# Kernel tuning notes

Measured on AMD Instinct MI355X. Metric: run time of the kernel, lower is better.

The kernel has to match this reference:

```python
import jax, jax.numpy as jnp
import numpy as np

NEG_SLOPE = 0.2  # PyG GATConv default leaky_relu slope


def _gat_layer(x, src, dst, n_nodes, W, a_src, a_dst, b, heads, out_ch):
    # x: [N, Fin] -> h: [N, H, C]
    h = (x @ W).reshape(n_nodes, heads, out_ch)
    alpha_s = jnp.einsum('nhc,hc->nh', h, a_src)  # [N, H]
    alpha_d = jnp.einsum('nhc,hc->nh', h, a_dst)  # [N, H]
    e = jax.nn.leaky_relu(alpha_s[src] + alpha_d[dst], NEG_SLOPE)  # [E, H]
    # segment softmax over edges grouped by destination node
    m = jax.ops.segment_max(e, dst, num_segments=n_nodes)          # [N, H]
    e = jnp.exp(e - m[dst])
    denom = jax.ops.segment_sum(e, dst, num_segments=n_nodes)      # [N, H]
    alpha = e / denom[dst]                                          # self-loops guarantee denom > 0
    msg = alpha[:, :, None] * h[src]                                # [E, H, C]
    out = jax.ops.segment_sum(msg, dst, num_segments=n_nodes)      # [N, H, C]
    return out.reshape(n_nodes, heads * out_ch) + b


def reference(x, edge_index, batch, W1, a_src1, a_dst1, b1, W2, a_src2, a_dst2, b2, fc_w, fc_b):
    n_nodes = x.shape[0]
    heads = a_src1.shape[0]
    # PyG GATConv adds self-loops by default
    loops = jnp.arange(n_nodes, dtype=edge_index.dtype)
    src = jnp.concatenate([edge_index[0], loops])
    dst = jnp.concatenate([edge_index[1], loops])

    h = _gat_layer(x, src, dst, n_nodes, W1, a_src1, a_dst1, b1, heads, 64)
    h = jax.nn.relu(h)  # dropout is identity in eval mode
    h = _gat_layer(h, src, dst, n_nodes, W2, a_src2, a_dst2, b2, heads, 16)
    h = jax.nn.relu(h)

    n_graphs = 64
    sums = jax.ops.segment_sum(h, batch, num_segments=n_graphs)                    # [G, 64]
    counts = jax.ops.segment_sum(jnp.ones((n_nodes,), h.dtype), batch, num_segments=n_graphs)
    pooled = sums / jnp.maximum(counts, 1.0)[:, None]                              # global_mean_pool
    return pooled @ fc_w + fc_b


def setup_inputs() -> dict:
    key = jax.random.key(0)
    ks = jax.random.split(key, 12)
    N, E, F_in, G = 50000, 800000, 128, 64
    H = 4
    x = jax.random.normal(ks[0], (N, F_in), jnp.float32)
    edge_index = jax.random.randint(ks[1], (2, E), 0, N, jnp.int32)
    batch = jnp.sort(jax.random.randint(ks[2], (N,), 0, G, jnp.int32))
    s1 = 1.0 / np.sqrt(F_in)
    s2 = 1.0 / np.sqrt(H * 64)
    s3 = 1.0 / np.sqrt(H * 16)
    return {
        'x': x,
        'edge_index': edge_index,
        'batch': batch,
        'W1': jax.random.normal(ks[3], (F_in, H * 64), jnp.float32) * s1,
        'a_src1': jax.random.normal(ks[4], (H, 64), jnp.float32) * s1,
        'a_dst1': jax.random.normal(ks[5], (H, 64), jnp.float32) * s1,
        'b1': jnp.zeros((H * 64,), jnp.float32),
        'W2': jax.random.normal(ks[6], (H * 64, H * 16), jnp.float32) * s2,
        'a_src2': jax.random.normal(ks[7], (H, 16), jnp.float32) * s2,
        'a_dst2': jax.random.normal(ks[8], (H, 16), jnp.float32) * s2,
        'b2': jnp.zeros((H * 16,), jnp.float32),
        'fc_w': jax.random.normal(ks[9], (H * 16, 32), jnp.float32) * s3,
        'fc_b': jnp.zeros((32,), jnp.float32),
    }
```

## Files before the change

### kernel.cpp

```cpp
#include <hip/hip_runtime.h>
#include <hip/hip_bf16.h>
#include <hip/hip_fp16.h>
#include <math.h>

#define HEADS 4
#define CAP 64
#define CS 16

typedef _Float16 half8_t __attribute__((ext_vector_type(8)));
typedef float float4_t __attribute__((ext_vector_type(4)));


__global__ __launch_bounds__(256) void prep_k(int* cnt, unsigned short* slots, int N, int NB,
                                              const float* __restrict__ W1, _Float16* __restrict__ W1T,
                                              const float* __restrict__ W2, _Float16* __restrict__ W2T) {
    int bx = blockIdx.x;
    if (bx < NB) {
        int i = bx * 256 + threadIdx.x;
        if (i < N) {
            cnt[(size_t)i * CS] = 1;
            slots[(size_t)i * CAP] = (unsigned short)i;
        }
    } else if (bx < NB + 128) {
        int k = bx - NB;
        int n = threadIdx.x;
        W1T[n * 128 + k] = (_Float16)W1[k * 256 + n];
    } else {
        int n = bx - NB - 128;
        int k = threadIdx.x;
        W2T[n * 256 + k] = (_Float16)W2[k * 64 + n];
    }
}


__global__ __launch_bounds__(256) void fused_scatter_gemm1_k(
    const int* __restrict__ src, const int* __restrict__ dst,
    int* __restrict__ cnt, unsigned short* __restrict__ slots, int E, int SB,
    const float* __restrict__ A,
    const _Float16* __restrict__ BT,
    __half* __restrict__ hout,
    const float* __restrict__ avs,
    const float* __restrict__ avd,
    float* __restrict__ os,
    float* __restrict__ od, int M) {
    __shared__ _Float16 lds[4 * 16 * 72];

    if ((int)blockIdx.x < SB) {
        int T = SB * 256;
        int t0 = blockIdx.x * 256 + threadIdx.x;
        int d[8], s[8];
        #pragma unroll
        for (int k = 0; k < 8; k++) {
            int i = t0 + k * T;
            if (i < E) { d[k] = dst[i]; s[k] = src[i]; }
            else d[k] = -1;
        }
        int p[8];
        #pragma unroll
        for (int k = 0; k < 8; k++) {
            if (d[k] >= 0) p[k] = atomicAdd(&cnt[(size_t)d[k] * CS], 1);
        }
        #pragma unroll
        for (int k = 0; k < 8; k++) {
            if (d[k] >= 0 && p[k] < CAP)
                slots[(size_t)d[k] * CAP + p[k]] = (unsigned short)s[k];
        }
        return;
    }

    int bx = blockIdx.x - SB;
    int wave = threadIdx.x >> 6;
    int lane = threadIdx.x & 63;
    int q = lane >> 4;
    int c16 = lane & 15;
    int row0 = bx * 64 + wave * 16;

    half8_t a[4];
    int ar = row0 + c16;
    bool avalid = (ar < M);
    const float* ap = A + (size_t)ar * 128;
    #pragma unroll
    for (int ks = 0; ks < 4; ks++) {
        if (avalid) {
            float4 f0 = *(const float4*)(ap + ks * 32 + q * 8);
            float4 f1 = *(const float4*)(ap + ks * 32 + q * 8 + 4);
            half8_t h;
            h[0] = (_Float16)f0.x; h[1] = (_Float16)f0.y;
            h[2] = (_Float16)f0.z; h[3] = (_Float16)f0.w;
            h[4] = (_Float16)f1.x; h[5] = (_Float16)f1.y;
            h[6] = (_Float16)f1.z; h[7] = (_Float16)f1.w;
            a[ks] = h;
        } else {
            a[ks] = (half8_t)(_Float16)0.0f;
        }
    }

    float4_t acc[16];
    #pragma unroll
    for (int ct = 0; ct < 16; ct++) acc[ct] = (float4_t)0.f;

    #pragma unroll
    for (int ks = 0; ks < 4; ks++) {
        #pragma unroll
        for (int ct = 0; ct < 16; ct++) {
            half8_t b = *(const half8_t*)(BT + (size_t)(ct * 16 + c16) * 128 + ks * 32 + q * 8);
            acc[ct] = __builtin_amdgcn_mfma_f32_16x16x32_f16(a[ks], b, acc[ct], 0, 0, 0);
        }
    }

    float psh[4][4] = {}, pdh[4][4] = {};
    #pragma unroll
    for (int ct = 0; ct < 16; ct++) {
        int h = ct >> 2;
        int cih = (ct & 3) * 16 + c16;
        float as_v = avs[h * 64 + cih];
        float ad_v = avd[h * 64 + cih];
        #pragma unroll
        for (int r = 0; r < 4; r++) {
            psh[h][r] = fmaf(acc[ct][r], as_v, psh[h][r]);
            pdh[h][r] = fmaf(acc[ct][r], ad_v, pdh[h][r]);
        }
    }
    #pragma unroll
    for (int h = 0; h < 4; h++) {
        #pragma unroll
        for (int r = 0; r < 4; r++) {
            #pragma unroll
            for (int o = 8; o >= 1; o >>= 1) {
                psh[h][r] += __shfl_down(psh[h][r], o, 16);
                pdh[h][r] += __shfl_down(pdh[h][r], o, 16);
            }
        }
    }
    if (c16 == 0) {
        #pragma unroll
        for (int r = 0; r < 4; r++) {
            int gr = row0 + q * 4 + r;
            if (gr < M) {
                #pragma unroll
                for (int h = 0; h < 4; h++) {
                    os[(size_t)gr * HEADS + h] = psh[h][r];
                    od[(size_t)gr * HEADS + h] = pdh[h][r];
                }
            }
        }
    }

    _Float16* wl = lds + wave * (16 * 72);
    #pragma unroll
    for (int chunk = 0; chunk < 4; chunk++) {
        #pragma unroll
        for (int c4 = 0; c4 < 4; c4++) {
            int ct = chunk * 4 + c4;
            #pragma unroll
            for (int r = 0; r < 4; r++) {
                wl[(q * 4 + r) * 72 + c4 * 16 + c16] = (_Float16)acc[ct][r];
            }
        }
        __syncthreads();
        #pragma unroll
        for (int pass = 0; pass < 2; pass++) {
            int idx8 = pass * 64 + lane;
            int row = idx8 >> 3;
            int col8 = idx8 & 7;
            int gr = row0 + row;
            if (gr < M) {
                *(half8_t*)(hout + (size_t)gr * 256 + chunk * 64 + col8 * 8) =
                    *(const half8_t*)(wl + row * 72 + col8 * 8);
            }
        }
        __syncthreads();
    }
}


__global__ __launch_bounds__(256) void mfma_gemm2_k(
    const _Float16* __restrict__ Ah,
    const _Float16* __restrict__ BT,
    __half* __restrict__ hout,
    const float* __restrict__ avs,
    const float* __restrict__ avd,
    float* __restrict__ os,
    float* __restrict__ od, int M) {
    __shared__ _Float16 lds[4 * 16 * 64];
    int wave = threadIdx.x >> 6;
    int lane = threadIdx.x & 63;
    int q = lane >> 4;
    int c16 = lane & 15;
    int row0 = blockIdx.x * 64 + wave * 16;

    half8_t a[8];
    int ar = row0 + c16;
    bool avalid = (ar < M);
    const _Float16* ap = Ah + (size_t)ar * 256;
    #pragma unroll
    for (int ks = 0; ks < 8; ks++) {
        if (avalid) a[ks] = *(const half8_t*)(ap + ks * 32 + q * 8);
        else        a[ks] = (half8_t)(_Float16)0.0f;
    }

    float4_t acc[4];
    #pragma unroll
    for (int ct = 0; ct < 4; ct++) acc[ct] = (float4_t)0.f;

    #pragma unroll
    for (int ks = 0; ks < 8; ks++) {
        #pragma unroll
        for (int ct = 0; ct < 4; ct++) {
            half8_t b = *(const half8_t*)(BT + (size_t)(ct * 16 + c16) * 256 + ks * 32 + q * 8);
            acc[ct] = __builtin_amdgcn_mfma_f32_16x16x32_f16(a[ks], b, acc[ct], 0, 0, 0);
        }
    }

    float ps[4][4], pd[4][4];
    #pragma unroll
    for (int ct = 0; ct < 4; ct++) {
        float as_v = avs[ct * 16 + c16];
        float ad_v = avd[ct * 16 + c16];
        #pragma unroll
        for (int r = 0; r < 4; r++) {
            ps[ct][r] = acc[ct][r] * as_v;
            pd[ct][r] = acc[ct][r] * ad_v;
            #pragma unroll
            for (int o = 8; o >= 1; o >>= 1) {
                ps[ct][r] += __shfl_down(ps[ct][r], o, 16);
                pd[ct][r] += __shfl_down(pd[ct][r], o, 16);
            }
        }
    }
    if (c16 == 0) {
        #pragma unroll
        for (int r = 0; r < 4; r++) {
            int gr = row0 + q * 4 + r;
            if (gr < M) {
                #pragma unroll
                for (int ct = 0; ct < 4; ct++) {
                    os[(size_t)gr * HEADS + ct] = ps[ct][r];
                    od[(size_t)gr * HEADS + ct] = pd[ct][r];
                }
            }
        }
    }

    _Float16* wl = lds + wave * (16 * 64);
    #pragma unroll
    for (int ct = 0; ct < 4; ct++) {
        #pragma unroll
        for (int r = 0; r < 4; r++) {
            wl[(q * 4 + r) * 64 + ct * 16 + c16] = (_Float16)acc[ct][r];
        }
    }
    __syncthreads();
    #pragma unroll
    for (int pass = 0; pass < 2; pass++) {
        int idx8 = pass * 64 + lane;
        int row = idx8 >> 3;
        int col8 = idx8 & 7;
        int gr = row0 + row;
        if (gr < M) {
            *(half8_t*)(hout + (size_t)gr * 64 + col8 * 8) =
                *(const half8_t*)(wl + row * 64 + col8 * 8);
        }
    }
}


__global__ __launch_bounds__(256) void gat_agg64_f16_k(
    const __half* __restrict__ hsrc,
    const float* __restrict__ as,
    const float* __restrict__ ad,
    const int* __restrict__ cnt,
    const unsigned short* __restrict__ slots,
    const float* __restrict__ bias,
    __half* __restrict__ outh,
    int N) {
    int node = blockIdx.x * 4 + (threadIdx.x >> 6);
    if (node >= N) return;
    int l = threadIdx.x & 63;
    int h = l >> 4;
    int je = l & 15;
    int hb = h << 4;
    int deg = min(cnt[(size_t)node * CS], CAP);
    const unsigned short* sp = slots + (size_t)node * CAP;
    float adh = ad[(size_t)node * HEADS + h];
    float4 bv = *(const float4*)(bias + l * 4);

    int sv[4];
    float ev[4];
    #pragma unroll
    for (int k = 0; k < 4; k++) {
        int j = k * 16 + je;
        sv[k] = (j < deg) ? (int)sp[j] : 0;
    }
    #pragma unroll
    for (int k = 0; k < 4; k++) {
        int j = k * 16 + je;
        if (j < deg) {
            float a = as[(size_t)sv[k] * HEADS + h] + adh;
            ev[k] = (a > 0.f) ? a : 0.2f * a;
        } else {
            ev[k] = -INFINITY;
        }
    }
    float m = fmaxf(fmaxf(ev[0], ev[1]), fmaxf(ev[2], ev[3]));
    #pragma unroll
    for (int o = 8; o >= 1; o >>= 1) m = fmaxf(m, __shfl_xor(m, o));
    float pv[4];
    float den = 0.f;
    #pragma unroll
    for (int k = 0; k < 4; k++) {
        pv[k] = (k * 16 + je < deg) ? __expf(ev[k] - m) : 0.f;
        den += pv[k];
    }
    #pragma unroll
    for (int o = 8; o >= 1; o >>= 1) den += __shfl_xor(den, o);

    float4 acc = make_float4(0.f, 0.f, 0.f, 0.f);
    #pragma unroll
    for (int k = 0; k < 4; k++) {
        int base = k * 16;
        if (base >= deg) break;
        int cl = min(16, deg - base);
        #pragma unroll
        for (int half = 0; half < 2; half++) {
            int j0 = half * 8;
            if (j0 >= cl) break;
            float pj[8]; int sj[8];
            #pragma unroll
            for (int jj = 0; jj < 8; jj++) {
                pj[jj] = __shfl(pv[k], hb + j0 + jj);
                sj[jj] = __shfl(sv[k], hb + j0 + jj);
            }
            uint2 rv[8];
            #pragma unroll
            for (int jj = 0; jj < 8; jj++) {
                if (j0 + jj < cl) rv[jj] = *(const uint2*)(hsrc + (size_t)sj[jj] * 256 + l * 4);
            }
            #pragma unroll
            for (int jj = 0; jj < 8; jj++) {
                if (j0 + jj < cl) {
                    float2 a0 = __half22float2(*(__half2*)&rv[jj].x);
                    float2 b0 = __half22float2(*(__half2*)&rv[jj].y);
                    acc.x = fmaf(pj[jj], a0.x, acc.x); acc.y = fmaf(pj[jj], a0.y, acc.y);
                    acc.z = fmaf(pj[jj], b0.x, acc.z); acc.w = fmaf(pj[jj], b0.y, acc.w);
                }
            }
        }
    }

    float inv = 1.f / den;
    float rx = fmaxf(fmaf(acc.x, inv, bv.x), 0.f);
    float ry = fmaxf(fmaf(acc.y, inv, bv.y), 0.f);
    float rz = fmaxf(fmaf(acc.z, inv, bv.z), 0.f);
    float rw = fmaxf(fmaf(acc.w, inv, bv.w), 0.f);
    __half2* op = (__half2*)(outh + (size_t)node * 256 + l * 4);
    op[0] = __floats2half2_rn(rx, ry);
    op[1] = __floats2half2_rn(rz, rw);
}


__global__ __launch_bounds__(256) void gat_agg16_f16_k(
    const __half* __restrict__ hsrc,
    const float* __restrict__ as,
    const float* __restrict__ ad,
    const int* __restrict__ cnt,
    const unsigned short* __restrict__ slots,
    const float* __restrict__ bias,
    float* __restrict__ out, int N) {
    int node = blockIdx.x * 4 + (threadIdx.x >> 6);
    if (node >= N) return;
    int l = threadIdx.x & 63;
    int ha = l >> 4;
    int je = l & 15;
    int q = l & 15;
    int hh = q >> 2;
    int eg = l >> 4;
    int deg = min(cnt[(size_t)node * CS], CAP);
    const unsigned short* sp = slots + (size_t)node * CAP;
    float adh = ad[(size_t)node * HEADS + ha];
    float m = -INFINITY, den = 0.f;
    float4 acc = make_float4(0.f, 0.f, 0.f, 0.f);
    for (int base = 0; base < deg; base += 16) {
        int cl = min(16, deg - base);
        int s = 0;
        float e = -INFINITY;
        if (je < cl) {
            s = sp[base + je];
            float a = as[(size_t)s * HEADS + ha] + adh;
            e = (a > 0.f) ? a : 0.2f * a;
        }
        float cmax = e;
        #pragma unroll
        for (int o = 8; o >= 1; o >>= 1) cmax = fmaxf(cmax, __shfl_xor(cmax, o));
        float m_new = fmaxf(m, cmax);
        float p = (je < cl) ? __expf(e - m_new) : 0.f;
        float sum = p;
        #pragma unroll
        for (int o = 8; o >= 1; o >>= 1) sum += __shfl_xor(sum, o);
        float sc = __expf(m - m_new);
        den = den * sc + sum;
        m = m_new;
        float sch = __shfl(sc, hh << 4);
        acc.x *= sch; acc.y *= sch; acc.z *= sch; acc.w *= sch;

        int jbase = eg * 4;
        float pj[4]; int sj[4]; bool vj[4];
        #pragma unroll
        for (int jj = 0; jj < 4; jj++) {
            int j = jbase + jj;
            int jc = min(j, cl - 1);
            pj[jj] = __shfl(p, (hh << 4) + jc);
            sj[jj] = __shfl(s, (hh << 4) + jc);
            vj[jj] = (j < cl);
        }
        uint2 rv[4];
        #pragma unroll
        for (int jj = 0; jj < 4; jj++) {
            if (vj[jj]) rv[jj] = *(const uint2*)(hsrc + (size_t)sj[jj] * 64 + q * 4);
        }
        #pragma unroll
        for (int jj = 0; jj < 4; jj++) {
            if (vj[jj]) {
                float2 f0 = __half22float2(*(__half2*)&rv[jj].x);
                float2 f1 = __half22float2(*(__half2*)&rv[jj].y);
                acc.x = fmaf(pj[jj], f0.x, acc.x); acc.y = fmaf(pj[jj], f0.y, acc.y);
                acc.z = fmaf(pj[jj], f1.x, acc.z); acc.w = fmaf(pj[jj], f1.y, acc.w);
            }
        }
    }
    acc.x += __shfl_xor(acc.x, 16); acc.y += __shfl_xor(acc.y, 16);
    acc.z += __shfl_xor(acc.z, 16); acc.w += __shfl_xor(acc.w, 16);
    acc.x += __shfl_xor(acc.x, 32); acc.y += __shfl_xor(acc.y, 32);
    acc.z += __shfl_xor(acc.z, 32); acc.w += __shfl_xor(acc.w, 32);
    float denh = __shfl(den, hh << 4);
    if (eg == 0) {
        float inv = 1.f / denh;
        float4 bv = *(const float4*)(bias + q * 4);
        float4 r;
        r.x = fmaxf(fmaf(acc.x, inv, bv.x), 0.f);
        r.y = fmaxf(fmaf(acc.y, inv, bv.y), 0.f);
        r.z = fmaxf(fmaf(acc.z, inv, bv.z), 0.f);
        r.w = fmaxf(fmaf(acc.w, inv, bv.w), 0.f);
        *(float4*)(out + (size_t)node * 64 + q * 4) = r;
    }
}


__global__ __launch_bounds__(256) void bounds_zero_k(const int* __restrict__ batch, int N,
                                                     int* __restrict__ bstart,
                                                     float* __restrict__ sums) {
    int t = threadIdx.x;
    if (t <= 64) {
        int lo = 0, hi = N;
        while (lo < hi) {
            int mid = (lo + hi) >> 1;
            if (batch[mid] < t) lo = mid + 1; else hi = mid;
        }
        bstart[t] = lo;
    }
    for (int i = t; i < 64 * 64; i += 256) sums[i] = 0.f;
}

__global__ __launch_bounds__(256) void pool_sum_k(const float* __restrict__ g2,
                                                  const int* __restrict__ batch,
                                                  float* __restrict__ sums, int N) {
    int c = threadIdx.x & 63;
    int r = threadIdx.x >> 6;
    int base = blockIdx.x * 256;
    int lim = min(base + 256, N);
    float acc = 0.f;
    int cur = -1;
    for (int n = base + r; n < lim; n += 4) {
        int g = batch[n];
        if (g != cur) {
            if (cur >= 0) atomicAdd(&sums[cur * 64 + c], acc);
            acc = 0.f;
            cur = g;
        }
        acc += g2[(size_t)n * 64 + c];
    }
    if (cur >= 0) atomicAdd(&sums[cur * 64 + c], acc);
}

__global__ void fc_k(const float* __restrict__ sums, const int* __restrict__ bstart,
                     const float* __restrict__ w, const float* __restrict__ b,
                     float* __restrict__ out) {
    int g = blockIdx.x, o = threadIdx.x;
    float cnt_ = (float)max(bstart[g + 1] - bstart[g], 1);
    float inv = 1.f / cnt_;
    float acc = b[o];
    for (int k = 0; k < 64; k++) acc = fmaf(sums[g * 64 + k] * inv, w[k * 32 + o], acc);
    out[g * 32 + o] = acc;
}


static inline size_t align_up(size_t x, size_t a) { return (x + a - 1) & ~(a - 1); }

extern "C" void kernel_launch(void* const* d_in, const int* in_sizes, int n_in,
                              void* d_out, int out_size, void* d_ws, size_t ws_size,
                              hipStream_t stream) {
    const float* x      = (const float*)d_in[0];
    const int*   ei     = (const int*)d_in[1];
    const int*   batch  = (const int*)d_in[2];
    const float* W1     = (const float*)d_in[3];
    const float* a_src1 = (const float*)d_in[4];
    const float* a_dst1 = (const float*)d_in[5];
    const float* b1     = (const float*)d_in[6];
    const float* W2     = (const float*)d_in[7];
    const float* a_src2 = (const float*)d_in[8];
    const float* a_dst2 = (const float*)d_in[9];
    const float* b2     = (const float*)d_in[10];
    const float* fc_w   = (const float*)d_in[11];
    const float* fc_b   = (const float*)d_in[12];
    float* out = (float*)d_out;

    const int N = in_sizes[2];
    const int E = in_sizes[1] / 2;
    const int F_in = in_sizes[0] / N;
    const int D1 = HEADS * 64;
    const int D2 = HEADS * 16;

    const int* src = ei;
    const int* dst = ei + E;

    char* w = (char*)d_ws;
    size_t off = 0;
    auto alloc = [&](size_t bytes) {
        size_t p = off;
        off = align_up(off + bytes, 256);
        return (void*)(w + p);
    };
    int* cnt    = (int*)alloc((size_t)N * CS * 4);
    unsigned short* slots = (unsigned short*)alloc((size_t)N * CAP * 2);
    int* bstart = (int*)alloc(65 * 4);
    float* pooled = (float*)alloc(64 * 64 * 4);
    float* as1  = (float*)alloc((size_t)N * HEADS * 4);
    float* ad1  = (float*)alloc((size_t)N * HEADS * 4);
    float* as2  = (float*)alloc((size_t)N * HEADS * 4);
    float* ad2  = (float*)alloc((size_t)N * HEADS * 4);
    __half* h1h = (__half*)alloc((size_t)N * D1 * 2);
    __half* g1h = (__half*)alloc((size_t)N * D1 * 2);
    __half* h2h = (__half*)alloc((size_t)N * D2 * 2);
    float* g2   = (float*)alloc((size_t)N * D2 * 4);
    _Float16* w1t = (_Float16*)alloc((size_t)F_in * D1 * 2);
    _Float16* w2t = (_Float16*)alloc((size_t)D1 * D2 * 2);

    const int NB = (N + 255) / 256;
    prep_k<<<NB + 128 + 64, 256, 0, stream>>>(cnt, slots, N, NB, W1, w1t, W2, w2t);

    const int SB = (E + 2047) / 2048;
    const int GB = (N + 63) / 64;
    fused_scatter_gemm1_k<<<SB + GB, 256, 0, stream>>>(
        src, dst, cnt, slots, E, SB,
        x, w1t, h1h, a_src1, a_dst1, as1, ad1, N);

    gat_agg64_f16_k<<<(N + 3) / 4, 256, 0, stream>>>(h1h, as1, ad1, cnt, slots, b1, g1h, N);

    mfma_gemm2_k<<<(N + 63) / 64, 256, 0, stream>>>((const _Float16*)g1h, w2t, h2h,
                                                    a_src2, a_dst2, as2, ad2, N);
    gat_agg16_f16_k<<<(N + 3) / 4, 256, 0, stream>>>(h2h, as2, ad2, cnt, slots, b2, g2, N);

    bounds_zero_k<<<1, 256, 0, stream>>>(batch, N, bstart, pooled);
    pool_sum_k<<<(N + 255) / 256, 256, 0, stream>>>(g2, batch, pooled, N);
    fc_k<<<64, 32, 0, stream>>>(pooled, bstart, fc_w, fc_b, out);
}
```

Before: 312.6 us.

## Fuse layer-1 aggregation with layer-2 GEMM through shared memory

Merges the 64-wide GAT aggregation kernel and the second MFMA GEMM into one kernel. Each block aggregates 16 nodes (4 per wave, processed sequentially) into an LDS tile, then each wave computes one 16-column tile of the layer-2 projection and attention logits. This removes the round trip of the N×256 fp16 intermediate through global memory and one launch. In exchange, each wave handles four nodes serially, so fewer independent gathers are in flight per block, and the h2 output stores are scalar halves rather than vectorized.

```diff
diff --git a/kernel.cpp b/kernel.cpp
--- a/kernel.cpp
+++ b/kernel.cpp
@@ -174,188 +174,153 @@
 }
 
 
-__global__ __launch_bounds__(256) void mfma_gemm2_k(
-    const _Float16* __restrict__ Ah,
-    const _Float16* __restrict__ BT,
-    __half* __restrict__ hout,
-    const float* __restrict__ avs,
-    const float* __restrict__ avd,
-    float* __restrict__ os,
-    float* __restrict__ od, int M) {
-    __shared__ _Float16 lds[4 * 16 * 64];
-    int wave = threadIdx.x >> 6;
-    int lane = threadIdx.x & 63;
-    int q = lane >> 4;
-    int c16 = lane & 15;
-    int row0 = blockIdx.x * 64 + wave * 16;
-
-    half8_t a[8];
-    int ar = row0 + c16;
-    bool avalid = (ar < M);
-    const _Float16* ap = Ah + (size_t)ar * 256;
-    #pragma unroll
-    for (int ks = 0; ks < 8; ks++) {
-        if (avalid) a[ks] = *(const half8_t*)(ap + ks * 32 + q * 8);
-        else        a[ks] = (half8_t)(_Float16)0.0f;
-    }
-
-    float4_t acc[4];
-    #pragma unroll
-    for (int ct = 0; ct < 4; ct++) acc[ct] = (float4_t)0.f;
-
-    #pragma unroll
-    for (int ks = 0; ks < 8; ks++) {
-        #pragma unroll
-        for (int ct = 0; ct < 4; ct++) {
-            half8_t b = *(const half8_t*)(BT + (size_t)(ct * 16 + c16) * 256 + ks * 32 + q * 8);
-            acc[ct] = __builtin_amdgcn_mfma_f32_16x16x32_f16(a[ks], b, acc[ct], 0, 0, 0);
-        }
-    }
-
-    float ps[4][4], pd[4][4];
-    #pragma unroll
-    for (int ct = 0; ct < 4; ct++) {
-        float as_v = avs[ct * 16 + c16];
-        float ad_v = avd[ct * 16 + c16];
-        #pragma unroll
-        for (int r = 0; r < 4; r++) {
-            ps[ct][r] = acc[ct][r] * as_v;
-            pd[ct][r] = acc[ct][r] * ad_v;
-            #pragma unroll
-            for (int o = 8; o >= 1; o >>= 1) {
-                ps[ct][r] += __shfl_down(ps[ct][r], o, 16);
-                pd[ct][r] += __shfl_down(pd[ct][r], o, 16);
-            }
-        }
-    }
-    if (c16 == 0) {
-        #pragma unroll
-        for (int r = 0; r < 4; r++) {
-            int gr = row0 + q * 4 + r;
-            if (gr < M) {
-                #pragma unroll
-                for (int ct = 0; ct < 4; ct++) {
-                    os[(size_t)gr * HEADS + ct] = ps[ct][r];
-                    od[(size_t)gr * HEADS + ct] = pd[ct][r];
-                }
-            }
-        }
-    }
-
-    _Float16* wl = lds + wave * (16 * 64);
-    #pragma unroll
-    for (int ct = 0; ct < 4; ct++) {
-        #pragma unroll
-        for (int r = 0; r < 4; r++) {
-            wl[(q * 4 + r) * 64 + ct * 16 + c16] = (_Float16)acc[ct][r];
-        }
-    }
-    __syncthreads();
-    #pragma unroll
-    for (int pass = 0; pass < 2; pass++) {
-        int idx8 = pass * 64 + lane;
-        int row = idx8 >> 3;
-        int col8 = idx8 & 7;
-        int gr = row0 + row;
-        if (gr < M) {
-            *(half8_t*)(hout + (size_t)gr * 64 + col8 * 8) =
-                *(const half8_t*)(wl + row * 64 + col8 * 8);
-        }
-    }
-}
-
-
-__global__ __launch_bounds__(256) void gat_agg64_f16_k(
+__global__ __launch_bounds__(256) void fused_agg64_gemm2_k(
     const __half* __restrict__ hsrc,
     const float* __restrict__ as,
     const float* __restrict__ ad,
     const int* __restrict__ cnt,
     const unsigned short* __restrict__ slots,
-    const float* __restrict__ bias,
-    __half* __restrict__ outh,
+    const float* __restrict__ bias1,
+    const _Float16* __restrict__ BT,
+    const float* __restrict__ avs2,
+    const float* __restrict__ avd2,
+    __half* __restrict__ h2out,
+    float* __restrict__ os2,
+    float* __restrict__ od2,
     int N) {
-    int node = blockIdx.x * 4 + (threadIdx.x >> 6);
-    if (node >= N) return;
-    int l = threadIdx.x & 63;
-    int h = l >> 4;
-    int je = l & 15;
+    __shared__ __align__(16) _Float16 g1t[16 * 264];
+
+    int wave = threadIdx.x >> 6;
+    int lane = threadIdx.x & 63;
+    int nb = blockIdx.x * 16;
+
+    int h = lane >> 4;
+    int je = lane & 15;
     int hb = h << 4;
-    int deg = min(cnt[(size_t)node * CS], CAP);
-    const unsigned short* sp = slots + (size_t)node * CAP;
-    float adh = ad[(size_t)node * HEADS + h];
-    float4 bv = *(const float4*)(bias + l * 4);
-
-    int sv[4];
-    float ev[4];
-    #pragma unroll
-    for (int k = 0; k < 4; k++) {
-        int j = k * 16 + je;
-        sv[k] = (j < deg) ? (int)sp[j] : 0;
-    }
-    #pragma unroll
-    for (int k = 0; k < 4; k++) {
-        int j = k * 16 + je;
-        if (j < deg) {
-            float a = as[(size_t)sv[k] * HEADS + h] + adh;
-            ev[k] = (a > 0.f) ? a : 0.2f * a;
-        } else {
-            ev[k] = -INFINITY;
-        }
-    }
-    float m = fmaxf(fmaxf(ev[0], ev[1]), fmaxf(ev[2], ev[3]));
-    #pragma unroll
-    for (int o = 8; o >= 1; o >>= 1) m = fmaxf(m, __shfl_xor(m, o));
-    float pv[4];
-    float den = 0.f;
-    #pragma unroll
-    for (int k = 0; k < 4; k++) {
-        pv[k] = (k * 16 + je < deg) ? __expf(ev[k] - m) : 0.f;
-        den += pv[k];
-    }
-    #pragma unroll
-    for (int o = 8; o >= 1; o >>= 1) den += __shfl_xor(den, o);
-
-    float4 acc = make_float4(0.f, 0.f, 0.f, 0.f);
-    #pragma unroll
-    for (int k = 0; k < 4; k++) {
-        int base = k * 16;
-        if (base >= deg) break;
-        int cl = min(16, deg - base);
-        #pragma unroll
-        for (int half = 0; half < 2; half++) {
-            int j0 = half * 8;
-            if (j0 >= cl) break;
-            float pj[8]; int sj[8];
+    float4 bv = *(const float4*)(bias1 + lane * 4);
+
+    for (int i = 0; i < 4; i++) {
+        int row = wave * 4 + i;
+        int node = nb + row;
+        _Float16* grow = g1t + row * 264;
+        __half2* gp = (__half2*)(grow + lane * 4);
+        if (node >= N) {
+            __half2 z = __floats2half2_rn(0.f, 0.f);
+            gp[0] = z; gp[1] = z;
+            continue;
+        }
+        int deg = min(cnt[(size_t)node * CS], CAP);
+        const unsigned short* sp = slots + (size_t)node * CAP;
+        float adh = ad[(size_t)node * HEADS + h];
+
+        int sv[4];
+        float ev[4];
+        #pragma unroll
+        for (int k = 0; k < 4; k++) {
+            int j = k * 16 + je;
+            sv[k] = (j < deg) ? (int)sp[j] : 0;
+        }
+        #pragma unroll
+        for (int k = 0; k < 4; k++) {
+            int j = k * 16 + je;
+            if (j < deg) {
+                float a = as[(size_t)sv[k] * HEADS + h] + adh;
+                ev[k] = (a > 0.f) ? a : 0.2f * a;
+            } else {
+                ev[k] = -INFINITY;
+            }
+        }
+        float m = fmaxf(fmaxf(ev[0], ev[1]), fmaxf(ev[2], ev[3]));
+        #pragma unroll
+        for (int o = 8; o >= 1; o >>= 1) m = fmaxf(m, __shfl_xor(m, o));
+        float pv[4];
+        float den = 0.f;
+        #pragma unroll
+        for (int k = 0; k < 4; k++) {
+            pv[k] = (k * 16 + je < deg) ? __expf(ev[k] - m) : 0.f;
+            den += pv[k];
+        }
+        #pragma unroll
+        for (int o = 8; o >= 1; o >>= 1) den += __shfl_xor(den, o);
+
+        float4 acc = make_float4(0.f, 0.f, 0.f, 0.f);
+        #pragma unroll
+        for (int k = 0; k < 4; k++) {
+            int base = k * 16;
+            if (base >= deg) break;
+            int cl = min(16, deg - base);
             #pragma unroll
-            for (int jj = 0; jj < 8; jj++) {
-                pj[jj] = __shfl(pv[k], hb + j0 + jj);
-                sj[jj] = __shfl(sv[k], hb + j0 + jj);
-            }
-            uint2 rv[8];
-            #pragma unroll
-            for (int jj = 0; jj < 8; jj++) {
-                if (j0 + jj < cl) rv[jj] = *(const uint2*)(hsrc + (size_t)sj[jj] * 256 + l * 4);
-            }
-            #pragma unroll
-            for (int jj = 0; jj < 8; jj++) {
-                if (j0 + jj < cl) {
-                    float2 a0 = __half22float2(*(__half2*)&rv[jj].x);
-                    float2 b0 = __half22float2(*(__half2*)&rv[jj].y);
-                    acc.x = fmaf(pj[jj], a0.x, acc.x); acc.y = fmaf(pj[jj], a0.y, acc.y);
-                    acc.z = fmaf(pj[jj], b0.x, acc.z); acc.w = fmaf(pj[jj], b0.y, acc.w);
+            for (int hf = 0; hf < 2; hf++) {
+                int j0 = hf * 8;
+                if (j0 >= cl) break;
+                float pj[8]; int sj[8];
+                #pragma unroll
+                for (int jj = 0; jj < 8; jj++) {
+                    pj[jj] = __shfl(pv[k], hb + j0 + jj);
+                    sj[jj] = __shfl(sv[k], hb + j0 + jj);
                 }
-            }
-        }
-    }
-
-    float inv = 1.f / den;
-    float rx = fmaxf(fmaf(acc.x, inv, bv.x), 0.f);
-    float ry = fmaxf(fmaf(acc.y, inv, bv.y), 0.f);
-    float rz = fmaxf(fmaf(acc.z, inv, bv.z), 0.f);
-    float rw = fmaxf(fmaf(acc.w, inv, bv.w), 0.f);
-    __half2* op = (__half2*)(outh + (size_t)node * 256 + l * 4);
-    op[0] = __floats2half2_rn(rx, ry);
-    op[1] = __floats2half2_rn(rz, rw);
+                uint2 rv[8];
+                #pragma unroll
+                for (int jj = 0; jj < 8; jj++) {
+                    if (j0 + jj < cl) rv[jj] = *(const uint2*)(hsrc + (size_t)sj[jj] * 256 + lane * 4);
+                }
+                #pragma unroll
+                for (int jj = 0; jj < 8; jj++) {
+                    if (j0 + jj < cl) {
+                        float2 a0 = __half22float2(*(__half2*)&rv[jj].x);
+                        float2 b0 = __half22float2(*(__half2*)&rv[jj].y);
+                        acc.x = fmaf(pj[jj], a0.x, acc.x); acc.y = fmaf(pj[jj], a0.y, acc.y);
+                        acc.z = fmaf(pj[jj], b0.x, acc.z); acc.w = fmaf(pj[jj], b0.y, acc.w);
+                    }
+                }
+            }
+        }
+
+        float inv = 1.f / den;
+        float rx = fmaxf(fmaf(acc.x, inv, bv.x), 0.f);
+        float ry = fmaxf(fmaf(acc.y, inv, bv.y), 0.f);
+        float rz = fmaxf(fmaf(acc.z, inv, bv.z), 0.f);
+        float rw = fmaxf(fmaf(acc.w, inv, bv.w), 0.f);
+        gp[0] = __floats2half2_rn(rx, ry);
+        gp[1] = __floats2half2_rn(rz, rw);
+    }
+    __syncthreads();
+
+    int q = lane >> 4;
+    int c16 = lane & 15;
+    int ct = wave;
+    float4_t acc2 = (float4_t)0.f;
+    #pragma unroll
+    for (int ks = 0; ks < 8; ks++) {
+        half8_t av = *(const half8_t*)(g1t + c16 * 264 + ks * 32 + q * 8);
+        half8_t bv8 = *(const half8_t*)(BT + (size_t)(ct * 16 + c16) * 256 + ks * 32 + q * 8);
+        acc2 = __builtin_amdgcn_mfma_f32_16x16x32_f16(av, bv8, acc2, 0, 0, 0);
+    }
+
+    float as_v = avs2[ct * 16 + c16];
+    float ad_v = avd2[ct * 16 + c16];
+    float ps[4], pd[4];
+    #pragma unroll
+    for (int r = 0; r < 4; r++) {
+        ps[r] = acc2[r] * as_v;
+        pd[r] = acc2[r] * ad_v;
+        #pragma unroll
+        for (int o = 8; o >= 1; o >>= 1) {
+            ps[r] += __shfl_down(ps[r], o, 16);
+            pd[r] += __shfl_down(pd[r], o, 16);
+        }
+    }
+    #pragma unroll
+    for (int r = 0; r < 4; r++) {
+        int gr = nb + q * 4 + r;
+        if (gr < N) {
+            h2out[(size_t)gr * 64 + ct * 16 + c16] = __float2half(acc2[r]);
+            if (c16 == 0) {
+                os2[(size_t)gr * HEADS + ct] = ps[r];
+                od2[(size_t)gr * HEADS + ct] = pd[r];
+            }
+        }
+    }
 }
 
 
@@ -539,7 +504,6 @@
     float* as2  = (float*)alloc((size_t)N * HEADS * 4);
     float* ad2  = (float*)alloc((size_t)N * HEADS * 4);
     __half* h1h = (__half*)alloc((size_t)N * D1 * 2);
-    __half* g1h = (__half*)alloc((size_t)N * D1 * 2);
     __half* h2h = (__half*)alloc((size_t)N * D2 * 2);
     float* g2   = (float*)alloc((size_t)N * D2 * 4);
     _Float16* w1t = (_Float16*)alloc((size_t)F_in * D1 * 2);
@@ -554,10 +518,10 @@
         src, dst, cnt, slots, E, SB,
         x, w1t, h1h, a_src1, a_dst1, as1, ad1, N);
 
-    gat_agg64_f16_k<<<(N + 3) / 4, 256, 0, stream>>>(h1h, as1, ad1, cnt, slots, b1, g1h, N);
-
-    mfma_gemm2_k<<<(N + 63) / 64, 256, 0, stream>>>((const _Float16*)g1h, w2t, h2h,
-                                                    a_src2, a_dst2, as2, ad2, N);
+    fused_agg64_gemm2_k<<<(N + 15) / 16, 256, 0, stream>>>(
+        h1h, as1, ad1, cnt, slots, b1,
+        w2t, a_src2, a_dst2, h2h, as2, ad2, N);
+
     gat_agg16_f16_k<<<(N + 3) / 4, 256, 0, stream>>>(h2h, as2, ad2, cnt, slots, b2, g2, N);
 
     bounds_zero_k<<<1, 256, 0, stream>>>(batch, N, bstart, pooled);
```

Result: no change. 309.0 us, median of 2 (-1.1%).
